# Kernel optimization log

Measured on AMD Instinct MI355X. Metric: run time of the kernel, lower is better.

The kernel has to match this reference:

```python
import jax, jax.numpy as jnp
import numpy as np

N_EMBD = 768
N_HEAD = 12
B, T = 2, 2048
EPS = 1e-5


def _layernorm(x, g, b):
    mu = jnp.mean(x, axis=-1, keepdims=True)
    var = jnp.var(x, axis=-1, keepdims=True)
    return (x - mu) * jax.lax.rsqrt(var + EPS) * g + b


def _mha(q, k, v, causal):
    # q,k,v: [B,T,C] already projected
    Bq, Tq, C = q.shape
    d = C // N_HEAD
    q = q.reshape(Bq, Tq, N_HEAD, d).transpose(0, 2, 1, 3)  # b h t d
    k = k.reshape(Bq, Tq, N_HEAD, d).transpose(0, 2, 1, 3)
    v = v.reshape(Bq, Tq, N_HEAD, d).transpose(0, 2, 1, 3)
    scores = jnp.einsum('bhqd,bhkd->bhqk', q, k) * (1.0 / jnp.sqrt(jnp.float32(d)))
    if causal:
        mask = jnp.tril(jnp.ones((Tq, Tq), dtype=bool))
        scores = jnp.where(mask[None, None], scores, jnp.float32(-jnp.inf))
    att = jax.nn.softmax(scores, axis=-1)
    y = jnp.einsum('bhqk,bhkd->bhqd', att, v)
    return y.transpose(0, 2, 1, 3).reshape(Bq, Tq, C)


def setup_inputs() -> dict:
    key = jax.random.key(0)
    ks = iter(jax.random.split(key, 32))
    C = N_EMBD

    def lin(kk, din, dout):
        w = jax.random.normal(kk, (din, dout), jnp.float32) * (1.0 / np.sqrt(din))
        return w

    inp = {
        'x': jax.random.normal(next(ks), (B, T, C), jnp.float32),
        'encoder_output': jax.random.normal(next(ks), (B, T, C), jnp.float32),
        'ln1_g': jnp.ones((C,), jnp.float32), 'ln1_b': jnp.zeros((C,), jnp.float32),
        'attn_qkv_w': lin(next(ks), C, 3 * C), 'attn_qkv_b': jnp.zeros((3 * C,), jnp.float32),
        'attn_proj_w': lin(next(ks), C, C), 'attn_proj_b': jnp.zeros((C,), jnp.float32),
        'ln2_g': jnp.ones((C,), jnp.float32), 'ln2_b': jnp.zeros((C,), jnp.float32),
        'ca_q_w': lin(next(ks), C, C), 'ca_q_b': jnp.zeros((C,), jnp.float32),
        'ca_k_w': lin(next(ks), C, C), 'ca_k_b': jnp.zeros((C,), jnp.float32),
        'ca_v_w': lin(next(ks), C, C), 'ca_v_b': jnp.zeros((C,), jnp.float32),
        'ca_o_w': lin(next(ks), C, C), 'ca_o_b': jnp.zeros((C,), jnp.float32),
        'ln3_g': jnp.ones((C,), jnp.float32), 'ln3_b': jnp.zeros((C,), jnp.float32),
        'fc_w': lin(next(ks), C, 4 * C), 'fc_b': jnp.zeros((4 * C,), jnp.float32),
        'fc2_w': lin(next(ks), 4 * C, C), 'fc2_b': jnp.zeros((C,), jnp.float32),
    }
    return inp


def reference(x, encoder_output, ln1_g, ln1_b, attn_qkv_w, attn_qkv_b,
              attn_proj_w, attn_proj_b, ln2_g, ln2_b,
              ca_q_w, ca_q_b, ca_k_w, ca_k_b, ca_v_w, ca_v_b, ca_o_w, ca_o_b,
              ln3_g, ln3_b, fc_w, fc_b, fc2_w, fc2_b):
    C = N_EMBD
    # causal self-attention
    qkv = x @ attn_qkv_w + attn_qkv_b
    q, k, v = qkv[..., :C], qkv[..., C:2 * C], qkv[..., 2 * C:]
    sa = _mha(q, k, v, causal=True) @ attn_proj_w + attn_proj_b
    x = _layernorm(sa + x, ln1_g, ln1_b)
    # cross-attention
    cq = x @ ca_q_w + ca_q_b
    ck = encoder_output @ ca_k_w + ca_k_b
    cv = encoder_output @ ca_v_w + ca_v_b
    ca = _mha(cq, ck, cv, causal=False) @ ca_o_w + ca_o_b
    x = _layernorm(ca + x, ln2_g, ln2_b)
    # MLP
    h = jax.nn.relu(x @ fc_w + fc_b) @ fc2_w + fc2_b
    x = _layernorm(h + x, ln3_g, ln3_b)
    return x
```

## Files before the change

### kernel.cpp

```cpp
#include <hip/hip_runtime.h>


#define C_EMBD 768
#define NHEAD  12
#define HD     64
#define TB     2048
#define BB     2
#define MTOK   (BB*TB)

typedef __bf16 bf16_8 __attribute__((ext_vector_type(8)));
typedef float  f32x4  __attribute__((ext_vector_type(4)));

#if __has_builtin(__builtin_amdgcn_exp2f)
#define EXP2(x) __builtin_amdgcn_exp2f(x)
#else
#define EXP2(x) exp2f(x)
#endif

__device__ __forceinline__ unsigned short f2bf(float f) {
    union { __bf16 h; unsigned short u; } c;
    c.h = (__bf16)f;
    return c.u;
}

#define GLOAD_LDS16(gsrc, ldst) \
    __builtin_amdgcn_global_load_lds( \
        (const __attribute__((address_space(1))) void*)(gsrc), \
        (__attribute__((address_space(3))) void*)(ldst), 16, 0, 0)

__global__ __launch_bounds__(256) void k_preproc(
        const float* __restrict__ x,     const float* __restrict__ enc,
        const float* __restrict__ qkv_w, const float* __restrict__ proj_w,
        const float* __restrict__ caq_w, const float* __restrict__ cak_w,
        const float* __restrict__ cav_w, const float* __restrict__ cao_w,
        const float* __restrict__ fc_w,  const float* __restrict__ fc2_w,
        const float* __restrict__ qkv_b, const float* __restrict__ caq_b,
        const float* __restrict__ cak_b, const float* __restrict__ cav_b,
        unsigned short* __restrict__ xbf,  unsigned short* __restrict__ encbf,
        unsigned short* __restrict__ wqkv, unsigned short* __restrict__ wproj,
        unsigned short* __restrict__ wcq,  unsigned short* __restrict__ wck,
        unsigned short* __restrict__ wcv,  unsigned short* __restrict__ wco,
        unsigned short* __restrict__ wfc,  unsigned short* __restrict__ wfc2,
        float* __restrict__ bqkv, float* __restrict__ bkv, float* __restrict__ bcq,
        float sc2) {
    __shared__ float tile[32][33];
    int b = blockIdx.x, tid = threadIdx.x;
    if (b < 9216) {
        const float* W; unsigned short* Wt; int K, N, t; float sc; int slim;
        if      (b < 1728) { W=qkv_w;  Wt=wqkv;  K=768;  N=2304; t=b;      sc=sc2; slim=768; }
        else if (b < 2304) { W=proj_w; Wt=wproj; K=768;  N=768;  t=b-1728; sc=1.f; slim=0;   }
        else if (b < 2880) { W=caq_w;  Wt=wcq;   K=768;  N=768;  t=b-2304; sc=sc2; slim=768; }
        else if (b < 3456) { W=cak_w;  Wt=wck;   K=768;  N=768;  t=b-2880; sc=1.f; slim=0;   }
        else if (b < 4032) { W=cav_w;  Wt=wcv;   K=768;  N=768;  t=b-3456; sc=1.f; slim=0;   }
        else if (b < 4608) { W=cao_w;  Wt=wco;   K=768;  N=768;  t=b-4032; sc=1.f; slim=0;   }
        else if (b < 6912) { W=fc_w;   Wt=wfc;   K=768;  N=3072; t=b-4608; sc=1.f; slim=0;   }
        else               { W=fc2_w;  Wt=wfc2;  K=3072; N=768;  t=b-6912; sc=1.f; slim=0;   }
        int ntx = N >> 5;
        int n0 = (t % ntx) * 32, k0 = (t / ntx) * 32;
        int tx = tid & 31, ty = tid >> 5;
#pragma unroll
        for (int i = 0; i < 4; ++i)
            tile[ty + 8*i][tx] = W[(size_t)(k0 + ty + 8*i) * N + n0 + tx];
        __syncthreads();
#pragma unroll
        for (int i = 0; i < 4; ++i) {
            int nrow = n0 + ty + 8*i;
            float s = (nrow < slim) ? sc : 1.0f;
            Wt[(size_t)nrow * K + k0 + tx] = f2bf(tile[tx][ty + 8*i] * s);
        }
    } else if (b < 15360) {
        int b2 = b - 9216;
        const float* src = (b2 < 3072) ? x   : enc;
        unsigned short* dst = (b2 < 3072) ? xbf : encbf;
        int i = (b2 < 3072 ? b2 : b2 - 3072) * 256 + tid;
        float4 v = ((const float4*)src)[i];
        ushort4 o;
        o.x = f2bf(v.x); o.y = f2bf(v.y); o.z = f2bf(v.z); o.w = f2bf(v.w);
        ((ushort4*)dst)[i] = o;
    } else {
        int b3 = b - 15360;
        if (b3 < 9) {
            int i = b3 * 256 + tid;
            if (i < 2304) bqkv[i] = qkv_b[i] * (i < 768 ? sc2 : 1.0f);
        } else if (b3 < 12) {
            int i = (b3 - 9) * 256 + tid;
            if (i < 768) { bkv[i] = cak_b[i]; bkv[768 + i] = cav_b[i]; }
        } else {
            int i = (b3 - 12) * 256 + tid;
            if (i < 768) bcq[i] = caq_b[i] * sc2;
        }
    }
}

template<int BM, bool OUT_BF16, bool ADD_RES, bool RELU>
__global__ __launch_bounds__(256) void k_gemm_bt(
        const unsigned short* __restrict__ A,
        const unsigned short* __restrict__ Bt,
        const float* __restrict__ bias,
        const float* __restrict__ res,
        void* __restrict__ Cout,
        int M, int N, int K) {
    constexpr int MF = BM / 32;
    __shared__ unsigned short As[BM * 32];
    __shared__ unsigned short Bs[128 * 32];
    int tid  = threadIdx.x;
    int lane = tid & 63, wave = tid >> 6;
    int l16 = lane & 15, lg = lane >> 4;
    int wm = (wave >> 1) * (BM / 2), wn = (wave & 1) * 64;
    int bm = blockIdx.x * BM, bn = blockIdx.y * 128;

    f32x4 acc[MF][4] = {};

    for (int k0 = 0; k0 < K; k0 += 32) {
        __syncthreads();
#pragma unroll
        for (int i = 0; i < BM / 64; ++i) {
            int chunk = i * 256 + tid;
            GLOAD_LDS16(A + (size_t)(bm + (chunk >> 2)) * K + k0 + (chunk & 3) * 8,
                        As + (size_t)(i * 256 + wave * 64) * 8);
        }
#pragma unroll
        for (int i = 0; i < 2; ++i) {
            int chunk = i * 256 + tid;
            GLOAD_LDS16(Bt + (size_t)(bn + (chunk >> 2)) * K + k0 + (chunk & 3) * 8,
                        Bs + (size_t)(i * 256 + wave * 64) * 8);
        }
        __syncthreads();
        bf16_8 af[MF], bfr[4];
#pragma unroll
        for (int m = 0; m < MF; ++m)
            af[m]  = *(const bf16_8*)(As + (size_t)(wm + m*16 + l16) * 32 + lg * 8);
#pragma unroll
        for (int n = 0; n < 4; ++n)
            bfr[n] = *(const bf16_8*)(Bs + (size_t)(wn + n*16 + l16) * 32 + lg * 8);
#pragma unroll
        for (int m = 0; m < MF; ++m)
#pragma unroll
            for (int n = 0; n < 4; ++n)
                acc[m][n] = __builtin_amdgcn_mfma_f32_16x16x32_bf16(af[m], bfr[n], acc[m][n], 0, 0, 0);
    }

#pragma unroll
    for (int m = 0; m < MF; ++m) {
#pragma unroll
        for (int n = 0; n < 4; ++n) {
            int col = bn + wn + n*16 + l16;
            float bv = bias[col];
#pragma unroll
            for (int r = 0; r < 4; ++r) {
                int row = bm + wm + m*16 + lg*4 + r;
                float v = acc[m][n][r] + bv;
                if (ADD_RES) v += res[(size_t)row * N + col];
                if (RELU)    v = fmaxf(v, 0.f);
                if (OUT_BF16) ((unsigned short*)Cout)[(size_t)row * N + col] = f2bf(v);
                else          ((float*)Cout)[(size_t)row * N + col] = v;
            }
        }
    }
}

template<bool CAUSAL>
__global__ __launch_bounds__(256) void k_attn(
        const unsigned short* __restrict__ Qp,
        const unsigned short* __restrict__ Kp,
        const unsigned short* __restrict__ Vp,
        unsigned short* __restrict__ Yp,
        int strideQ, int strideKV) {
    __shared__ __bf16 Ks[2][64][72];
    __shared__ __bf16 Vt[2][64][72];
    __shared__ __bf16 Ps[4][16][72];
    int tid  = threadIdx.x;
    int lane = tid & 63, wave = tid >> 6;
    int l16 = lane & 15, lg = lane >> 4;
    int bh = blockIdx.y;
    int b = bh / NHEAD, h = bh - b * NHEAD;
    int qt = CAUSAL ? (gridDim.x - 1 - blockIdx.x) : blockIdx.x;
    int wq = qt * 64 + wave * 16;

    const unsigned short* Qb = Qp + (size_t)b * TB * strideQ  + h * HD;
    const unsigned short* Kb = Kp + (size_t)b * TB * strideKV + h * HD;
    const unsigned short* Vb = Vp + (size_t)b * TB * strideKV + h * HD;

    bf16_8 qf0 = *(const bf16_8*)(Qb + (size_t)(wq + l16) * strideQ + lg * 8);
    bf16_8 qf1 = *(const bf16_8*)(Qb + (size_t)(wq + l16) * strideQ + 32 + lg * 8);

    bf16_8 vones;
#pragma unroll
    for (int j = 0; j < 8; ++j) vones[j] = (__bf16)1.0f;

    int kr = tid >> 3, kc = (tid & 7) * 8;
    int vk2 = (tid & 31) * 2;
    int vd0 = (tid >> 5) * 8;
    const size_t stepKV = (size_t)64 * strideKV;

    const unsigned short* gK0 = Kb + (size_t)kr  * strideKV + kc;
    const unsigned short* gK1 = gK0 + (size_t)32 * strideKV;
    const unsigned short* gV0 = Vb + (size_t)vk2 * strideKV + vd0;
    const unsigned short* gV1 = gV0 + strideKV;

    int4 kA = *(const int4*)gK0;
    int4 kB = *(const int4*)gK1;
    unsigned vp[8];
    {
        int4 va = *(const int4*)gV0, vb2 = *(const int4*)gV1;
        const unsigned short* pa = (const unsigned short*)&va;
        const unsigned short* pb = (const unsigned short*)&vb2;
#pragma unroll
        for (int j = 0; j < 8; ++j) vp[j] = (unsigned)pa[j] | ((unsigned)pb[j] << 16);
    }
    *(int4*)(&Ks[0][kr][kc])      = kA;
    *(int4*)(&Ks[0][kr + 32][kc]) = kB;
#pragma unroll
    for (int j = 0; j < 8; ++j)
        *(unsigned*)(&Vt[0][vd0 + j][vk2]) = vp[j];
    __syncthreads();

    f32x4 o[4] = {};
    float m_run[4], l_run[4];
#pragma unroll
    for (int r = 0; r < 4; ++r) { m_run[r] = -1e30f; l_run[r] = 0.f; }

    int ktEnd = CAUSAL ? (qt + 1) : (TB / 64);
    for (int kt = 0; kt < ktEnd; ++kt) {
        int cur = kt & 1;
        bool more = (kt + 1 < ktEnd);
        if (more) {
            gK0 += stepKV; gK1 += stepKV; gV0 += stepKV; gV1 += stepKV;
            kA = *(const int4*)gK0;
            kB = *(const int4*)gK1;
            int4 va = *(const int4*)gV0, vb2 = *(const int4*)gV1;
            const unsigned short* pa = (const unsigned short*)&va;
            const unsigned short* pb = (const unsigned short*)&vb2;
#pragma unroll
            for (int j = 0; j < 8; ++j) vp[j] = (unsigned)pa[j] | ((unsigned)pb[j] << 16);
        }

        f32x4 s[4];
#pragma unroll
        for (int n = 0; n < 4; ++n) {
            f32x4 z = {};
            bf16_8 kf0 = *(const bf16_8*)(&Ks[cur][n*16 + l16][lg*8]);
            bf16_8 kf1 = *(const bf16_8*)(&Ks[cur][n*16 + l16][32 + lg*8]);
            z = __builtin_amdgcn_mfma_f32_16x16x32_bf16(qf0, kf0, z, 0, 0, 0);
            z = __builtin_amdgcn_mfma_f32_16x16x32_bf16(qf1, kf1, z, 0, 0, 0);
            s[n] = z;
        }
        if (CAUSAL && kt == qt) {
#pragma unroll
            for (int n = 0; n < 4; ++n)
#pragma unroll
                for (int r = 0; r < 4; ++r)
                    if (kt*64 + n*16 + l16 > wq + lg*4 + r) s[n][r] = -1e30f;
        }
        float mx[4];
#pragma unroll
        for (int r = 0; r < 4; ++r)
            mx[r] = fmaxf(fmaxf(s[0][r], s[1][r]), fmaxf(s[2][r], s[3][r]));
#pragma unroll
        for (int off = 1; off < 16; off <<= 1)
#pragma unroll
            for (int r = 0; r < 4; ++r)
                mx[r] = fmaxf(mx[r], __shfl_xor(mx[r], off, 64));
        bool big = (mx[0] > m_run[0] + 8.f) | (mx[1] > m_run[1] + 8.f) |
                   (mx[2] > m_run[2] + 8.f) | (mx[3] > m_run[3] + 8.f);
        if (__any(big)) {
#pragma unroll
            for (int r = 0; r < 4; ++r) {
                float mnew = fmaxf(m_run[r], mx[r]);
                float sf = EXP2(m_run[r] - mnew);
                m_run[r] = mnew;
                l_run[r] *= sf;
#pragma unroll
                for (int n = 0; n < 4; ++n) o[n][r] *= sf;
            }
        }
#pragma unroll
        for (int n = 0; n < 4; ++n)
#pragma unroll
            for (int r = 0; r < 4; ++r)
                Ps[wave][lg*4 + r][n*16 + l16] = (__bf16)EXP2(s[n][r] - m_run[r]);

        f32x4 zsum = {};
#pragma unroll
        for (int kk = 0; kk < 2; ++kk) {
            bf16_8 pa = *(const bf16_8*)(&Ps[wave][l16][kk*32 + lg*8]);
            zsum = __builtin_amdgcn_mfma_f32_16x16x32_bf16(pa, vones, zsum, 0, 0, 0);
#pragma unroll
            for (int n = 0; n < 4; ++n) {
                bf16_8 vf = *(const bf16_8*)(&Vt[cur][n*16 + l16][kk*32 + lg*8]);
                o[n] = __builtin_amdgcn_mfma_f32_16x16x32_bf16(pa, vf, o[n], 0, 0, 0);
            }
        }
#pragma unroll
        for (int r = 0; r < 4; ++r) l_run[r] += zsum[r];

        if (more) {
            *(int4*)(&Ks[cur ^ 1][kr][kc])      = kA;
            *(int4*)(&Ks[cur ^ 1][kr + 32][kc]) = kB;
#pragma unroll
            for (int j = 0; j < 8; ++j)
                *(unsigned*)(&Vt[cur ^ 1][vd0 + j][vk2]) = vp[j];
        }
        __syncthreads();
    }

#pragma unroll
    for (int r = 0; r < 4; ++r) {
        float rl = 1.0f / l_run[r];
        int token = b * TB + wq + lg*4 + r;
#pragma unroll
        for (int n = 0; n < 4; ++n)
            Yp[(size_t)token * C_EMBD + h * HD + n*16 + l16] = f2bf(o[n][r] * rl);
    }
}

template<bool WF32, bool WBF16>
__global__ __launch_bounds__(256) void k_ln(const float* __restrict__ in,
                                            const float* __restrict__ g,
                                            const float* __restrict__ bb,
                                            float* __restrict__ outf,
                                            unsigned short* __restrict__ outb) {
    int row = blockIdx.x;
    const float* x = in + (size_t)row * C_EMBD;
    float v[3], s1 = 0.f, s2 = 0.f;
#pragma unroll
    for (int i = 0; i < 3; ++i) {
        v[i] = x[threadIdx.x + i * 256];
        s1 += v[i];
        s2 += v[i] * v[i];
    }
#pragma unroll
    for (int off = 1; off < 64; off <<= 1) {
        s1 += __shfl_xor(s1, off, 64);
        s2 += __shfl_xor(s2, off, 64);
    }
    __shared__ float red[8];
    int wave = threadIdx.x >> 6, lane = threadIdx.x & 63;
    if (lane == 0) { red[wave] = s1; red[4 + wave] = s2; }
    __syncthreads();
    s1 = red[0] + red[1] + red[2] + red[3];
    s2 = red[4] + red[5] + red[6] + red[7];
    float mu  = s1 * (1.f / C_EMBD);
    float var = s2 * (1.f / C_EMBD) - mu * mu;
    float rs  = rsqrtf(var + 1e-5f);
#pragma unroll
    for (int i = 0; i < 3; ++i) {
        int c = threadIdx.x + i * 256;
        float y = (v[i] - mu) * rs * g[c] + bb[c];
        if (WF32)  outf[(size_t)row * C_EMBD + c] = y;
        if (WBF16) outb[(size_t)row * C_EMBD + c] = f2bf(y);
    }
}

extern "C" void kernel_launch(void* const* d_in, const int* in_sizes, int n_in,
                              void* d_out, int out_size, void* d_ws, size_t ws_size,
                              hipStream_t stream) {
    (void)in_sizes; (void)n_in; (void)out_size; (void)ws_size;
    const float* x      = (const float*)d_in[0];
    const float* enc    = (const float*)d_in[1];
    const float* ln1_g  = (const float*)d_in[2];
    const float* ln1_b  = (const float*)d_in[3];
    const float* qkv_w  = (const float*)d_in[4];
    const float* qkv_b  = (const float*)d_in[5];
    const float* proj_w = (const float*)d_in[6];
    const float* proj_b = (const float*)d_in[7];
    const float* ln2_g  = (const float*)d_in[8];
    const float* ln2_b  = (const float*)d_in[9];
    const float* caq_w  = (const float*)d_in[10];
    const float* caq_b  = (const float*)d_in[11];
    const float* cak_w  = (const float*)d_in[12];
    const float* cak_b  = (const float*)d_in[13];
    const float* cav_w  = (const float*)d_in[14];
    const float* cav_b  = (const float*)d_in[15];
    const float* cao_w  = (const float*)d_in[16];
    const float* cao_b  = (const float*)d_in[17];
    const float* ln3_g  = (const float*)d_in[18];
    const float* ln3_b  = (const float*)d_in[19];
    const float* fc_w   = (const float*)d_in[20];
    const float* fc_b   = (const float*)d_in[21];
    const float* fc2_w  = (const float*)d_in[22];
    const float* fc2_b  = (const float*)d_in[23];
    float* out = (float*)d_out;

    char* ws = (char*)d_ws;
    auto us = [&](size_t off) { return (unsigned short*)(ws + off); };
    auto fl = [&](size_t off) { return (float*)(ws + off); };

    const size_t O_WQKV  = 0;
    const size_t O_WPROJ = 3538944;
    const size_t O_WCQ   = 4718592;
    const size_t O_WCK   = 5898240;
    const size_t O_WCV   = 7077888;
    const size_t O_WCO   = 8257536;
    const size_t O_WFC   = 9437184;
    const size_t O_WFC2  = 14155776;
    const size_t O_XBF   = 18874368;
    const size_t O_ENCBF = 25165824;
    const size_t O_QKVBF = 31457280;
    const size_t O_Q2    = O_QKVBF;
    const size_t O_KV2   = O_QKVBF + 6291456;
    const size_t O_YBF   = 50331648;
    const size_t O_RESF  = 56623104;
    const size_t O_X1F   = 69206016;
    const size_t O_X1BF  = 81788928;
    const size_t O_X2F   = 88080384;
    const size_t O_X2BF  = 100663296;
    const size_t O_HBF   = 106954752;
    const size_t O_BKV   = O_HBF;
    const size_t O_BQKV  = O_HBF + 8192;
    const size_t O_BCQ   = O_HBF + 20480;

    const float SC2 = 0.125f * 1.44269504f;

    k_preproc<<<15375, 256, 0, stream>>>(
        x, enc, qkv_w, proj_w, caq_w, cak_w, cav_w, cao_w, fc_w, fc2_w,
        qkv_b, caq_b, cak_b, cav_b,
        us(O_XBF), us(O_ENCBF),
        us(O_WQKV), us(O_WPROJ), us(O_WCQ), us(O_WCK),
        us(O_WCV), us(O_WCO), us(O_WFC), us(O_WFC2),
        fl(O_BQKV), fl(O_BKV), fl(O_BCQ), SC2);

    k_gemm_bt<128, true,  false, false><<<dim3(32, 18), 256, 0, stream>>>(
        us(O_XBF), us(O_WQKV), fl(O_BQKV), nullptr, us(O_QKVBF), MTOK, 2304, 768);
    k_attn<true><<<dim3(TB/64, BB*NHEAD), 256, 0, stream>>>(
        us(O_QKVBF), us(O_QKVBF) + 768, us(O_QKVBF) + 1536, us(O_YBF), 2304, 2304);
    k_gemm_bt<64, false, true,  false><<<dim3(64, 6), 256, 0, stream>>>(
        us(O_YBF), us(O_WPROJ), proj_b, x, fl(O_RESF), MTOK, 768, 768);
    k_ln<true, true><<<MTOK, 256, 0, stream>>>(fl(O_RESF), ln1_g, ln1_b, fl(O_X1F), us(O_X1BF));
    k_gemm_bt<64, true,  false, false><<<dim3(64, 6), 256, 0, stream>>>(
        us(O_X1BF),  us(O_WCQ), fl(O_BCQ), nullptr, us(O_Q2), MTOK, 768, 768);
    k_gemm_bt<128, true,  false, false><<<dim3(32, 12), 256, 0, stream>>>(
        us(O_ENCBF), us(O_WCK), fl(O_BKV), nullptr, us(O_KV2), MTOK, 1536, 768);
    k_attn<false><<<dim3(TB/64, BB*NHEAD), 256, 0, stream>>>(
        us(O_Q2), us(O_KV2), us(O_KV2) + 768, us(O_YBF), 768, 1536);
    k_gemm_bt<64, false, true,  false><<<dim3(64, 6), 256, 0, stream>>>(
        us(O_YBF), us(O_WCO), cao_b, fl(O_X1F), fl(O_RESF), MTOK, 768, 768);
    k_ln<true, true><<<MTOK, 256, 0, stream>>>(fl(O_RESF), ln2_g, ln2_b, fl(O_X2F), us(O_X2BF));
    k_gemm_bt<128, true,  false, true ><<<dim3(32, 24), 256, 0, stream>>>(
        us(O_X2BF), us(O_WFC), fc_b, nullptr, us(O_HBF), MTOK, 3072, 768);
    k_gemm_bt<64, false, true,  false><<<dim3(64, 6), 256, 0, stream>>>(
        us(O_HBF), us(O_WFC2), fc2_b, fl(O_X2F), fl(O_RESF), MTOK, 768, 3072);
    k_ln<true, false><<<MTOK, 256, 0, stream>>>(fl(O_RESF), ln3_g, ln3_b, out, nullptr);
}
```

Baseline: 502.3 us.

## Merge self-attn QKV and cross-attn KV GEMMs into one launch; shrink N=768 tiles

The QKV projection of x and the K/V projection of the encoder output now run in a single dual-problem kernel launch of 30 column blocks. The cross-attention KV buffer moves into the X2F region so it is not overwritten by later writes. The GEMM is generalised to template BM/BN/BK, and the N=768 GEMMs switch to 64x64 tiles, doubling their block count to 768 so more of the GPU's CUs are filled. Smaller tiles give less operand reuse per block, and O_KV2 aliasing X2F relies on X2F not being written until LN2, which runs after the cross-attention.

```diff
diff --git a/kernel.cpp b/kernel.cpp
--- a/kernel.cpp
+++ b/kernel.cpp
@@ -92,58 +92,62 @@
     }
 }
 
-template<int BM, bool OUT_BF16, bool ADD_RES, bool RELU>
-__global__ __launch_bounds__(256) void k_gemm_bt(
+template<int BM, int BN, int BK, bool OUT_BF16, bool ADD_RES, bool RELU>
+__device__ __forceinline__ void gemm_body(
+        unsigned short* As, unsigned short* Bs, int bm, int bn,
         const unsigned short* __restrict__ A,
         const unsigned short* __restrict__ Bt,
         const float* __restrict__ bias,
         const float* __restrict__ res,
         void* __restrict__ Cout,
-        int M, int N, int K) {
-    constexpr int MF = BM / 32;
-    __shared__ unsigned short As[BM * 32];
-    __shared__ unsigned short Bs[128 * 32];
+        int N, int K) {
+    constexpr int MF  = BM / 32, NF = BN / 32;
+    constexpr int ACH = BM * BK / 8 / 256;
+    constexpr int BCH = BN * BK / 8 / 256;
+    constexpr int CPR = BK / 8;
     int tid  = threadIdx.x;
     int lane = tid & 63, wave = tid >> 6;
     int l16 = lane & 15, lg = lane >> 4;
-    int wm = (wave >> 1) * (BM / 2), wn = (wave & 1) * 64;
-    int bm = blockIdx.x * BM, bn = blockIdx.y * 128;
-
-    f32x4 acc[MF][4] = {};
-
-    for (int k0 = 0; k0 < K; k0 += 32) {
+    int wm = (wave >> 1) * (BM / 2), wn = (wave & 1) * (BN / 2);
+
+    f32x4 acc[MF][NF] = {};
+
+    for (int k0 = 0; k0 < K; k0 += BK) {
         __syncthreads();
 #pragma unroll
-        for (int i = 0; i < BM / 64; ++i) {
+        for (int i = 0; i < ACH; ++i) {
             int chunk = i * 256 + tid;
-            GLOAD_LDS16(A + (size_t)(bm + (chunk >> 2)) * K + k0 + (chunk & 3) * 8,
+            GLOAD_LDS16(A + (size_t)(bm + chunk / CPR) * K + k0 + (chunk % CPR) * 8,
                         As + (size_t)(i * 256 + wave * 64) * 8);
         }
 #pragma unroll
-        for (int i = 0; i < 2; ++i) {
+        for (int i = 0; i < BCH; ++i) {
             int chunk = i * 256 + tid;
-            GLOAD_LDS16(Bt + (size_t)(bn + (chunk >> 2)) * K + k0 + (chunk & 3) * 8,
+            GLOAD_LDS16(Bt + (size_t)(bn + chunk / CPR) * K + k0 + (chunk % CPR) * 8,
                         Bs + (size_t)(i * 256 + wave * 64) * 8);
         }
         __syncthreads();
-        bf16_8 af[MF], bfr[4];
-#pragma unroll
-        for (int m = 0; m < MF; ++m)
-            af[m]  = *(const bf16_8*)(As + (size_t)(wm + m*16 + l16) * 32 + lg * 8);
-#pragma unroll
-        for (int n = 0; n < 4; ++n)
-            bfr[n] = *(const bf16_8*)(Bs + (size_t)(wn + n*16 + l16) * 32 + lg * 8);
-#pragma unroll
-        for (int m = 0; m < MF; ++m)
-#pragma unroll
-            for (int n = 0; n < 4; ++n)
-                acc[m][n] = __builtin_amdgcn_mfma_f32_16x16x32_bf16(af[m], bfr[n], acc[m][n], 0, 0, 0);
+#pragma unroll
+        for (int kk = 0; kk < BK / 32; ++kk) {
+            bf16_8 af[MF], bfr[NF];
+#pragma unroll
+            for (int m = 0; m < MF; ++m)
+                af[m]  = *(const bf16_8*)(As + (size_t)(wm + m*16 + l16) * BK + kk*32 + lg * 8);
+#pragma unroll
+            for (int n = 0; n < NF; ++n)
+                bfr[n] = *(const bf16_8*)(Bs + (size_t)(wn + n*16 + l16) * BK + kk*32 + lg * 8);
+#pragma unroll
+            for (int m = 0; m < MF; ++m)
+#pragma unroll
+                for (int n = 0; n < NF; ++n)
+                    acc[m][n] = __builtin_amdgcn_mfma_f32_16x16x32_bf16(af[m], bfr[n], acc[m][n], 0, 0, 0);
+        }
     }
 
 #pragma unroll
     for (int m = 0; m < MF; ++m) {
 #pragma unroll
-        for (int n = 0; n < 4; ++n) {
+        for (int n = 0; n < NF; ++n) {
             int col = bn + wn + n*16 + l16;
             float bv = bias[col];
 #pragma unroll
@@ -157,6 +161,34 @@
             }
         }
     }
+}
+
+template<int BM, int BN, int BK, bool OUT_BF16, bool ADD_RES, bool RELU>
+__global__ __launch_bounds__(256) void k_gemm_bt(
+        const unsigned short* __restrict__ A,
+        const unsigned short* __restrict__ Bt,
+        const float* __restrict__ bias,
+        const float* __restrict__ res,
+        void* __restrict__ Cout,
+        int N, int K) {
+    __shared__ unsigned short As[BM * BK];
+    __shared__ unsigned short Bs[BN * BK];
+    gemm_body<BM, BN, BK, OUT_BF16, ADD_RES, RELU>(
+        As, Bs, blockIdx.x * BM, blockIdx.y * BN, A, Bt, bias, res, Cout, N, K);
+}
+
+__global__ __launch_bounds__(256) void k_gemm_dual(
+        const unsigned short* __restrict__ A1, const unsigned short* __restrict__ B1,
+        const float* __restrict__ b1, unsigned short* __restrict__ o1,
+        const unsigned short* __restrict__ A2, const unsigned short* __restrict__ B2,
+        const float* __restrict__ b2, unsigned short* __restrict__ o2) {
+    __shared__ unsigned short As[128 * 32];
+    __shared__ unsigned short Bs[128 * 32];
+    const unsigned short *A, *Bt; const float* bias; unsigned short* out; int N, bn;
+    if (blockIdx.y < 18) { A = A1; Bt = B1; bias = b1; out = o1; N = 2304; bn = blockIdx.y * 128; }
+    else                 { A = A2; Bt = B2; bias = b2; out = o2; N = 1536; bn = (blockIdx.y - 18) * 128; }
+    gemm_body<128, 128, 32, true, false, false>(
+        As, Bs, blockIdx.x * 128, bn, A, Bt, bias, nullptr, out, N, 768);
 }
 
 template<bool CAUSAL>
@@ -398,12 +430,12 @@
     const size_t O_ENCBF = 25165824;
     const size_t O_QKVBF = 31457280;
     const size_t O_Q2    = O_QKVBF;
-    const size_t O_KV2   = O_QKVBF + 6291456;
     const size_t O_YBF   = 50331648;
     const size_t O_RESF  = 56623104;
     const size_t O_X1F   = 69206016;
     const size_t O_X1BF  = 81788928;
     const size_t O_X2F   = 88080384;
+    const size_t O_KV2   = O_X2F;
     const size_t O_X2BF  = 100663296;
     const size_t O_HBF   = 106954752;
     const size_t O_BKV   = O_HBF;
@@ -420,25 +452,24 @@
         us(O_WCV), us(O_WCO), us(O_WFC), us(O_WFC2),
         fl(O_BQKV), fl(O_BKV), fl(O_BCQ), SC2);
 
-    k_gemm_bt<128, true,  false, false><<<dim3(32, 18), 256, 0, stream>>>(
-        us(O_XBF), us(O_WQKV), fl(O_BQKV), nullptr, us(O_QKVBF), MTOK, 2304, 768);
+    k_gemm_dual<<<dim3(32, 30), 256, 0, stream>>>(
+        us(O_XBF),   us(O_WQKV), fl(O_BQKV), us(O_QKVBF),
+        us(O_ENCBF), us(O_WCK),  fl(O_BKV),  us(O_KV2));
     k_attn<true><<<dim3(TB/64, BB*NHEAD), 256, 0, stream>>>(
         us(O_QKVBF), us(O_QKVBF) + 768, us(O_QKVBF) + 1536, us(O_YBF), 2304, 2304);
-    k_gemm_bt<64, false, true,  false><<<dim3(64, 6), 256, 0, stream>>>(
-        us(O_YBF), us(O_WPROJ), proj_b, x, fl(O_RESF), MTOK, 768, 768);
+    k_gemm_bt<64, 64, 32, false, true,  false><<<dim3(64, 12), 256, 0, stream>>>(
+        us(O_YBF), us(O_WPROJ), proj_b, x, fl(O_RESF), 768, 768);
     k_ln<true, true><<<MTOK, 256, 0, stream>>>(fl(O_RESF), ln1_g, ln1_b, fl(O_X1F), us(O_X1BF));
-    k_gemm_bt<64, true,  false, false><<<dim3(64, 6), 256, 0, stream>>>(
-        us(O_X1BF),  us(O_WCQ), fl(O_BCQ), nullptr, us(O_Q2), MTOK, 768, 768);
-    k_gemm_bt<128, true,  false, false><<<dim3(32, 12), 256, 0, stream>>>(
-        us(O_ENCBF), us(O_WCK), fl(O_BKV), nullptr, us(O_KV2), MTOK, 1536, 768);
+    k_gemm_bt<64, 64, 32, true,  false, false><<<dim3(64, 12), 256, 0, stream>>>(
+        us(O_X1BF), us(O_WCQ), fl(O_BCQ), nullptr, us(O_Q2), 768, 768);
     k_attn<false><<<dim3(TB/64, BB*NHEAD), 256, 0, stream>>>(
         us(O_Q2), us(O_KV2), us(O_KV2) + 768, us(O_YBF), 768, 1536);
-    k_gemm_bt<64, false, true,  false><<<dim3(64, 6), 256, 0, stream>>>(
-        us(O_YBF), us(O_WCO), cao_b, fl(O_X1F), fl(O_RESF), MTOK, 768, 768);
+    k_gemm_bt<64, 64, 32, false, true,  false><<<dim3(64, 12), 256, 0, stream>>>(
+        us(O_YBF), us(O_WCO), cao_b, fl(O_X1F), fl(O_RESF), 768, 768);
     k_ln<true, true><<<MTOK, 256, 0, stream>>>(fl(O_RESF), ln2_g, ln2_b, fl(O_X2F), us(O_X2BF));
-    k_gemm_bt<128, true,  false, true ><<<dim3(32, 24), 256, 0, stream>>>(
-        us(O_X2BF), us(O_WFC), fc_b, nullptr, us(O_HBF), MTOK, 3072, 768);
-    k_gemm_bt<64, false, true,  false><<<dim3(64, 6), 256, 0, stream>>>(
-        us(O_HBF), us(O_WFC2), fc2_b, fl(O_X2F), fl(O_RESF), MTOK, 768, 3072);
+    k_gemm_bt<128, 128, 32, true,  false, true ><<<dim3(32, 24), 256, 0, stream>>>(
+        us(O_X2BF), us(O_WFC), fc_b, nullptr, us(O_HBF), 3072, 768);
+    k_gemm_bt<64, 64, 32, false, true,  false><<<dim3(64, 12), 256, 0, stream>>>(
+        us(O_HBF), us(O_WFC2), fc2_b, fl(O_X2F), fl(O_RESF), 768, 3072);
     k_ln<true, false><<<MTOK, 256, 0, stream>>>(fl(O_RESF), ln3_g, ln3_b, out, nullptr);
 }
```

After: 474.2 us. 1.06x faster.
